# Performance work log

Hardware: AMD Instinct MI355X
Metric: run time of the kernel (lower is better)

Reference implementation:

```python
import jax, jax.numpy as jnp
import numpy as np

N = 50000      # nodes
E = 1600000    # edges (before self loops)
IN = 128       # in_channels
HID = 64       # hidden_channels
HEADS = 2
NEG_SLOPE = 0.2  # PyG GATConv default


def setup_inputs() -> dict:
    key = jax.random.key(0)
    ks = jax.random.split(key, 12)
    s = 0.05
    return {
        "x": jax.random.normal(ks[0], (N, IN), jnp.float32),
        "edge_index": jax.random.randint(ks[1], (2, E), 0, N, dtype=jnp.int32),
        # layer 1: GATConv(IN -> HID, heads=HEADS, concat=True)
        "W1": jax.random.normal(ks[2], (IN, HEADS * HID), jnp.float32) * s,
        "a_src1": jax.random.normal(ks[3], (HEADS, HID), jnp.float32) * s,
        "a_dst1": jax.random.normal(ks[4], (HEADS, HID), jnp.float32) * s,
        "b1": jax.random.normal(ks[5], (HEADS * HID,), jnp.float32) * s,
        # layer 2: GATConv(HEADS*HID -> HID, heads=1, concat=False)
        "W2": jax.random.normal(ks[6], (HEADS * HID, HID), jnp.float32) * s,
        "a_src2": jax.random.normal(ks[7], (1, HID), jnp.float32) * s,
        "a_dst2": jax.random.normal(ks[8], (1, HID), jnp.float32) * s,
        "b2": jax.random.normal(ks[9], (HID,), jnp.float32) * s,
        "lin_w": jax.random.normal(ks[10], (HID, 1), jnp.float32) * s,
        "lin_b": jax.random.normal(ks[11], (1,), jnp.float32) * s,
    }


def gat_layer(x, src, dst, W, a_src, a_dst, b, heads, out_ch, concat, n):
    # linear transform: [n, heads, out_ch]
    h = (x @ W).reshape(n, heads, out_ch)
    # per-node attention logit halves  [n, heads]
    al_src = jnp.sum(h * a_src, axis=-1)
    al_dst = jnp.sum(h * a_dst, axis=-1)
    # per-edge logits (gather) + LeakyReLU  [e, heads]
    e = jax.nn.leaky_relu(al_src[src] + al_dst[dst], negative_slope=NEG_SLOPE)
    # segment softmax over edges grouped by destination node
    m = jax.ops.segment_max(e, dst, num_segments=n)
    ex = jnp.exp(e - m[dst])
    denom = jax.ops.segment_sum(ex, dst, num_segments=n)
    alpha = ex / (denom[dst] + 1e-16)
    # weighted message scatter-add  [n, heads, out_ch]
    out = jax.ops.segment_sum(h[src] * alpha[:, :, None], dst, num_segments=n)
    out = out.reshape(n, heads * out_ch) if concat else out.mean(axis=1)
    return out + b


def reference(x, edge_index, W1, a_src1, a_dst1, b1, W2, a_src2, a_dst2, b2, lin_w, lin_b):
    # PyG GATConv adds self loops by default
    loops = jnp.arange(N, dtype=edge_index.dtype)
    src = jnp.concatenate([edge_index[0], loops])
    dst = jnp.concatenate([edge_index[1], loops])
    h = gat_layer(x, src, dst, W1, a_src1, a_dst1, b1, HEADS, HID, True, N)
    h = jax.nn.elu(h)
    h = gat_layer(h, src, dst, W2, a_src2, a_dst2, b2, 1, HID, False, N)
    return (h @ lin_w + lin_b)[:, 0]  # squeeze(-1) -> [N]
```

## Files before the change

kernel.cpp:

```cpp
#include <hip/hip_runtime.h>
#include <hip/hip_fp16.h>


#define LEAKY(x) ((x) > 0.f ? (x) : 0.2f * (x))

typedef float v2f __attribute__((ext_vector_type(2)));
typedef _Float16 f16x8 __attribute__((ext_vector_type(8)));
typedef __fp16 h16x2 __attribute__((ext_vector_type(2)));
typedef float f32x4 __attribute__((ext_vector_type(4)));


template <int VPT>
__global__ __launch_bounds__(256) void bucket_cnt_kernel(const int* __restrict__ ei, int E, int n,
                                                         int* __restrict__ bc) {
  __shared__ int lc[256];
  int t = threadIdx.x;
  lc[t] = 0;
  __syncthreads();
  int base = blockIdx.x * (256 * VPT) + t;
  int tot = E + n;
#pragma unroll
  for (int u = 0; u < VPT; ++u) {
    int i = base + u * 256;
    if (i < tot) {
      int d = (i < E) ? ei[E + i] : (i - E);
      atomicAdd(&lc[d >> 8], 1);
    }
  }
  __syncthreads();
  if (lc[t]) atomicAdd(&bc[t], lc[t]);
}

__global__ __launch_bounds__(256) void bucket_scan_kernel(const int* __restrict__ bc,
                                                          int* __restrict__ boff,
                                                          int* __restrict__ bcur, int B,
                                                          int* __restrict__ off, int n, int Etot) {
  __shared__ int sm[256];
  int t = threadIdx.x;
  int v = (t < B) ? bc[t] : 0;
  sm[t] = v;
  __syncthreads();
  for (int s = 1; s < 256; s <<= 1) {
    int a = (t >= s) ? sm[t - s] : 0;
    __syncthreads();
    sm[t] += a;
    __syncthreads();
  }
  int excl = sm[t] - v;
  if (t < B) { boff[t] = excl; bcur[t] = excl; }
  if (t == 0) { boff[B] = Etot; off[n] = Etot; }
}

template <int VPT>
__global__ __launch_bounds__(256) void bucket_scatter_kernel(const int* __restrict__ ei, int E,
                                                             int n, int* __restrict__ bcur,
                                                             unsigned* __restrict__ entries) {
  __shared__ int lc[256];
  __shared__ int lbase[256];
  int t = threadIdx.x;
  lc[t] = 0;
  __syncthreads();
  int base = blockIdx.x * (256 * VPT) + t;
  int tot = E + n;
  int bb[VPT], ll[VPT];
  unsigned pk[VPT];
#pragma unroll
  for (int u = 0; u < VPT; ++u) {
    int i = base + u * 256;
    bb[u] = -1;
    if (i < tot) {
      int s, d;
      if (i < E) { s = ei[i]; d = ei[E + i]; }
      else       { s = d = i - E; }
      int b = d >> 8;
      bb[u] = b;
      ll[u] = atomicAdd(&lc[b], 1);
      pk[u] = (unsigned)s | ((unsigned)(d & 255) << 16);
    }
  }
  __syncthreads();
  if (lc[t]) lbase[t] = atomicAdd(&bcur[t], lc[t]);
  __syncthreads();
#pragma unroll
  for (int u = 0; u < VPT; ++u)
    if (bb[u] >= 0) entries[lbase[bb[u]] + ll[u]] = pk[u];
}

__global__ __launch_bounds__(256) void csr_build_kernel(const unsigned* __restrict__ entries,
                                                        const int* __restrict__ boff,
                                                        int* __restrict__ off,
                                                        unsigned* __restrict__ epair, int n) {
  __shared__ int hist[256];
  __shared__ int scn[256];
  __shared__ int cur[256];
  int b = blockIdx.x, t = threadIdx.x;
  int k0 = boff[b], k1 = boff[b + 1];
  hist[t] = 0;
  __syncthreads();
  for (int k = k0 + t; k < k1; k += 256) atomicAdd(&hist[(entries[k] >> 16) & 255], 1);
  __syncthreads();
  int v = hist[t];
  scn[t] = v;
  __syncthreads();
  for (int s = 1; s < 256; s <<= 1) {
    int a = (t >= s) ? scn[t - s] : 0;
    __syncthreads();
    scn[t] += a;
    __syncthreads();
  }
  int excl = scn[t] - v;
  int d = (b << 8) + t;
  if (d < n) off[d] = k0 + excl;
  cur[t] = k0 + excl;
  __syncthreads();
  unsigned dbase = (unsigned)(b << 8) << 16;
  for (int k = k0 + t; k < k1; k += 256) {
    unsigned e = entries[k];
    unsigned dl = (e >> 16) & 255;
    int p = atomicAdd(&cur[dl], 1);
    epair[p] = (e & 0xffffu) | (dbase + (dl << 16));
  }
}


__global__ __launch_bounds__(256) void wprep_kernel(const float* __restrict__ W1,
                                                    const float* __restrict__ W2,
                                                    const float* __restrict__ as2,
                                                    const float* __restrict__ ad2,
                                                    const float* __restrict__ lw,
                                                    unsigned short* __restrict__ Wp1,
                                                    float* __restrict__ vsrc2,
                                                    float* __restrict__ vdst2,
                                                    float* __restrict__ vlin) {
  int t = blockIdx.x * 256 + threadIdx.x;
  if (t < 16384) {
    int e = t;
    int i = e & 7;
    int c = (e >> 3) & 15;
    int g = (e >> 7) & 3;
    int kk = (e >> 9) & 3;
    int cn = e >> 11;
    int k = kk * 32 + g * 8 + i;
    int col = cn * 16 + c;
    __half h = __float2half(W1[k * 128 + col]);
    Wp1[e] = *(unsigned short*)&h;
  } else if (t < 16384 + 128) {
    int k = t - 16384;
    float a = 0.f, b = 0.f, s = 0.f;
    for (int cc = 0; cc < 64; ++cc) {
      float w = W2[k * 64 + cc];
      a = fmaf(w, as2[cc], a);
      b = fmaf(w, ad2[cc], b);
      s = fmaf(w, lw[cc], s);
    }
    vsrc2[k] = a;
    vdst2[k] = b;
    vlin[k] = s;
  }
}


__global__ __launch_bounds__(256) void gemm1_kernel(const float* __restrict__ X,
                                                    const uint4* __restrict__ Wp,
                                                    const float* __restrict__ a_src,
                                                    const float* __restrict__ a_dst,
                                                    unsigned char* __restrict__ Hout,
                                                    float2* __restrict__ als,
                                                    float2* __restrict__ ald, int n) {
  __shared__ float Xl[32 * 132];
  __shared__ float lgt[2][2][2][16];
  int t = threadIdx.x;
  int wave = t >> 6, lane = t & 63;
  int wm = wave >> 1, wn = wave & 1;
  int g = lane >> 4, c = lane & 15;
  int nb0 = blockIdx.x * 32;

  {
    const float4* Xg = (const float4*)X;
    float4* Xs = (float4*)Xl;
#pragma unroll
    for (int u = 0; u < 4; ++u) {
      int idx = u * 256 + t;
      int r = idx >> 5, c4 = idx & 31;
      int row = nb0 + r;
      int rc = row < n ? row : (n - 1);
      Xs[r * 33 + c4] = Xg[(size_t)rc * 32 + c4];
    }
  }
  __syncthreads();

  f16x8 af[4];
  const float* xr = Xl + (wm * 16 + c) * 132 + g * 8;
#pragma unroll
  for (int kk = 0; kk < 4; ++kk) {
    float4 x0 = *(const float4*)(xr + kk * 32);
    float4 x1 = *(const float4*)(xr + kk * 32 + 4);
    union { f16x8 v; h16x2 p[4]; } A;
    A.p[0] = __builtin_amdgcn_cvt_pkrtz(x0.x, x0.y);
    A.p[1] = __builtin_amdgcn_cvt_pkrtz(x0.z, x0.w);
    A.p[2] = __builtin_amdgcn_cvt_pkrtz(x1.x, x1.y);
    A.p[3] = __builtin_amdgcn_cvt_pkrtz(x1.z, x1.w);
    af[kk] = A.v;
  }

  f32x4 acc[4];
  f32x4 z = {0.f, 0.f, 0.f, 0.f};
#pragma unroll
  for (int cn = 0; cn < 4; ++cn) acc[cn] = z;
#pragma unroll
  for (int cn = 0; cn < 4; ++cn) {
    int cng = wn * 4 + cn;
#pragma unroll
    for (int kk = 0; kk < 4; ++kk) {
      union { uint4 u; f16x8 v; } B;
      B.u = Wp[(cng * 4 + kk) * 64 + lane];
      acc[cn] = __builtin_amdgcn_mfma_f32_16x16x32_f16(af[kk], B.v, acc[cn], 0, 0, 0);
    }
  }

  float asv[4], adv[4];
#pragma unroll
  for (int cn = 0; cn < 4; ++cn) {
    int col_l = wn * 64 + cn * 16 + c;
    asv[cn] = a_src[col_l];
    adv[cn] = a_dst[col_l];
  }
  float ps[4] = {0.f, 0.f, 0.f, 0.f};
  float pd[4] = {0.f, 0.f, 0.f, 0.f};
#pragma unroll
  for (int cn = 0; cn < 4; ++cn) {
#pragma unroll
    for (int r = 0; r < 4; ++r) {
      float v = acc[cn][r];
      ps[r] = fmaf(v, asv[cn], ps[r]);
      pd[r] = fmaf(v, adv[cn], pd[r]);
      int noder = nb0 + wm * 16 + g * 4 + r;
      int colg = wn * 64 + cn * 16 + c;
      if (noder < n) {
        int b8 = __builtin_amdgcn_cvt_pk_fp8_f32(v, v, 0, false);
        Hout[(size_t)noder * 128 + colg] = (unsigned char)(b8 & 0xff);
      }
    }
  }
#pragma unroll
  for (int r = 0; r < 4; ++r) {
#pragma unroll
    for (int m = 1; m <= 8; m <<= 1) {
      ps[r] += __shfl_xor(ps[r], m, 64);
      pd[r] += __shfl_xor(pd[r], m, 64);
    }
  }
  if (c == 0) {
#pragma unroll
    for (int r = 0; r < 4; ++r) {
      lgt[wm][wn][0][g * 4 + r] = ps[r];
      lgt[wm][wn][1][g * 4 + r] = pd[r];
    }
  }
  __syncthreads();
  if (t < 32) {
    int wmm = t >> 4, row = t & 15;
    int node = nb0 + wmm * 16 + row;
    if (node < n) {
      als[node] = make_float2(lgt[wmm][0][0][row], lgt[wmm][1][0][row]);
      ald[node] = make_float2(lgt[wmm][0][1][row], lgt[wmm][1][1][row]);
    }
  }
}


__global__ __launch_bounds__(256) void agg1_kernel(const unsigned char* __restrict__ Hb8,
                                                   const float2* __restrict__ als,
                                                   const float2* __restrict__ ald,
                                                   const unsigned* __restrict__ epair,
                                                   const int* __restrict__ off,
                                                   const float* __restrict__ b1,
                                                   const float* __restrict__ vsrc2,
                                                   const float* __restrict__ vdst2,
                                                   const float* __restrict__ vlin,
                                                   float2* __restrict__ gsrc,
                                                   float* __restrict__ adst2, int n) {
  __shared__ float wlds[4][128];
  int wid = (blockIdx.x * 256 + threadIdx.x) >> 6;
  int lane = threadIdx.x & 63;
  if (wid >= n) return;
  wid = __builtin_amdgcn_readfirstlane(wid);
  int wslot = (threadIdx.x >> 6) & 3;
  int half = lane >> 5;
  int k0 = off[wid], k1 = off[wid + 1];
  const unsigned short* Hu = (const unsigned short*)Hb8;
  float2 advv = ald[wid];
  float* wrow = &wlds[wslot][half << 6];

  float ax = 0.f, ay = 0.f, den = 0.f;

  for (int kb = k0; kb < k1; kb += 64) {
    int rem = min(k1 - kb, 64);
    int e = kb + (lane < rem ? lane : rem - 1);
    unsigned pp = epair[e];
    float2 l = als[pp & 0xffffu];
    float g0 = __expf(LEAKY(l.x + advv.x));
    float g1 = __expf(LEAKY(l.y + advv.y));
    wlds[wslot][lane] = g0;
    wlds[wslot][64 + lane] = g1;

#define EDGE1(jj)                                                                   \
  {                                                                                 \
    unsigned p = ((unsigned)__builtin_amdgcn_readlane((int)pp, (jj))) & 0xffffu;    \
    float w = wrow[(jj)];                                                           \
    unsigned short hv = Hu[(p << 6) | (unsigned)lane];                              \
    v2f hf = __builtin_amdgcn_cvt_pk_f32_fp8((int)hv, false);                       \
    den += w;                                                                       \
    ax = fmaf(hf.x, w, ax);                                                         \
    ay = fmaf(hf.y, w, ay);                                                         \
  }

    int nb = rem >> 3;
    for (int b = 0; b < nb; ++b) {
      int jb = b << 3;
#pragma unroll
      for (int j = 0; j < 8; ++j) EDGE1(jb + j);
    }
    for (int jj = nb << 3; jj < rem; ++jj) EDGE1(jj);
#undef EDGE1
  }

  float inv = 1.f / (den + 1e-16f);
  float2 bv = ((const float2*)b1)[lane];
  float r0 = ax * inv + bv.x;
  float r1 = ay * inv + bv.y;
  r0 = r0 > 0.f ? r0 : (__expf(r0) - 1.f);
  r1 = r1 > 0.f ? r1 : (__expf(r1) - 1.f);
  float2 vs = ((const float2*)vsrc2)[lane];
  float2 vd = ((const float2*)vdst2)[lane];
  float2 vl = ((const float2*)vlin)[lane];
  float ps = r0 * vs.x + r1 * vs.y;
  float pd = r0 * vd.x + r1 * vd.y;
  float sv = r0 * vl.x + r1 * vl.y;
#pragma unroll
  for (int m = 1; m <= 32; m <<= 1) {
    ps += __shfl_xor(ps, m, 64);
    pd += __shfl_xor(pd, m, 64);
    sv += __shfl_xor(sv, m, 64);
  }
  if (lane == 0) {
    gsrc[wid] = make_float2(ps, sv);
    adst2[wid] = pd;
  }
}

__global__ __launch_bounds__(256) void agg2_kernel(const float2* __restrict__ gsrc,
                                                   const float* __restrict__ adst2,
                                                   const unsigned* __restrict__ epair,
                                                   const int* __restrict__ off,
                                                   const float* __restrict__ b2,
                                                   const float* __restrict__ lin_w,
                                                   const float* __restrict__ lin_b,
                                                   float* __restrict__ out, int n) {
  int wid = (blockIdx.x * 256 + threadIdx.x) >> 6;
  int lane = threadIdx.x & 63;
  if (wid >= n) return;
  wid = __builtin_amdgcn_readfirstlane(wid);
  int k0 = off[wid], k1 = off[wid + 1];
  float adv = adst2[wid];

  float num = 0.f, den = 0.f;
  for (int kb = k0; kb < k1; kb += 64) {
    int e = kb + lane;
    bool ok = e < k1;
    unsigned pp = epair[ok ? e : k0];
    float2 g = gsrc[pp & 0xffffu];
    float w = ok ? __expf(LEAKY(g.x + adv)) : 0.f;
    num = fmaf(w, g.y, num);
    den += w;
  }
  float bt = b2[lane] * lin_w[lane];
#pragma unroll
  for (int m = 1; m <= 32; m <<= 1) {
    num += __shfl_xor(num, m, 64);
    den += __shfl_xor(den, m, 64);
    bt  += __shfl_xor(bt, m, 64);
  }
  if (lane == 0) out[wid] = num / (den + 1e-16f) + bt + lin_b[0];
}


static inline size_t alignup(size_t v) { return (v + 255) & ~(size_t)255; }

extern "C" void kernel_launch(void* const* d_in, const int* in_sizes, int n_in,
                              void* d_out, int out_size, void* d_ws, size_t ws_size,
                              hipStream_t stream) {
  const float* x   = (const float*)d_in[0];
  const int*   ei  = (const int*)d_in[1];
  const float* W1  = (const float*)d_in[2];
  const float* as1 = (const float*)d_in[3];
  const float* ad1 = (const float*)d_in[4];
  const float* b1  = (const float*)d_in[5];
  const float* W2  = (const float*)d_in[6];
  const float* as2 = (const float*)d_in[7];
  const float* ad2 = (const float*)d_in[8];
  const float* b2  = (const float*)d_in[9];
  const float* lw  = (const float*)d_in[10];
  const float* lb  = (const float*)d_in[11];
  float* out = (float*)d_out;

  const int N = out_size;
  const int E = in_sizes[1] / 2;
  const int Etot = E + N;
  const int B = (N + 255) >> 8;

  char* p = (char*)d_ws;
  int* bcnt = (int*)p;  p += alignup((size_t)(B + 1) * 4);
  int* boff = (int*)p;  p += alignup((size_t)(B + 1) * 4);
  int* bcur = (int*)p;  p += alignup((size_t)B * 4);
  unsigned* entries = (unsigned*)p; p += alignup((size_t)Etot * 4);
  int* off  = (int*)p;  p += alignup((size_t)(N + 1) * 4);
  unsigned* epair = (unsigned*)p; p += alignup((size_t)Etot * 4);
  float2* als = (float2*)p; p += alignup((size_t)N * 8);
  float2* ald = (float2*)p; p += alignup((size_t)N * 8);
  float2* gsrc = (float2*)p; p += alignup((size_t)N * 8);
  float* adst2 = (float*)p; p += alignup((size_t)N * 4);
  unsigned char* h1b = (unsigned char*)p; p += alignup((size_t)N * 128);
  unsigned short* wp1 = (unsigned short*)p; p += alignup((size_t)16384 * 2);
  float* vsrc2 = (float*)p; p += alignup((size_t)128 * 4);
  float* vdst2 = (float*)p; p += alignup((size_t)128 * 4);
  float* vlin  = (float*)p; p += alignup((size_t)128 * 4);

  hipMemsetAsync(bcnt, 0, (size_t)(B + 1) * sizeof(int), stream);

  constexpr int VPT = 8;
  int egrid = (Etot + 256 * VPT - 1) / (256 * VPT);

  wprep_kernel<<<65, 256, 0, stream>>>(W1, W2, as2, ad2, lw, wp1, vsrc2, vdst2, vlin);
  bucket_cnt_kernel<VPT><<<egrid, 256, 0, stream>>>(ei, E, N, bcnt);
  bucket_scan_kernel<<<1, 256, 0, stream>>>(bcnt, boff, bcur, B, off, N, Etot);
  bucket_scatter_kernel<VPT><<<egrid, 256, 0, stream>>>(ei, E, N, bcur, entries);
  csr_build_kernel<<<B, 256, 0, stream>>>(entries, boff, off, epair, N);

  gemm1_kernel<<<(N + 31) / 32, 256, 0, stream>>>(
      x, (const uint4*)wp1, as1, ad1, h1b, als, ald, N);
  agg1_kernel<<<(N + 3) / 4, 256, 0, stream>>>(h1b, als, ald, epair, off, b1,
                                               vsrc2, vdst2, vlin, gsrc, adst2, N);
  agg2_kernel<<<(N + 3) / 4, 256, 0, stream>>>(gsrc, adst2, epair, off, b2, lw, lb, out, N);
}
```

Measured before the change: 152.7 us.

## Build CSR with global per-node atomics and 16-bit source indices

Replaces the two-level bucket sort (bucket count, bucket scatter, per-bucket CSR build) with a direct per-destination histogram using global atomics, a three-stage scan for offsets, and an atomic-cursor scatter. The edge list now stores only 16-bit source indices, which halves the edge array read by both aggregation kernels and removes one full pass over the edges. The cost is heavy contention on global atomics across about 1.65M edges spread over 50K counters, plus an extra launch. Edge order within each node becomes nondeterministic, which can change floating-point summation order.

```diff
diff --git a/kernel.cpp b/kernel.cpp
--- a/kernel.cpp
+++ b/kernel.cpp
@@ -11,33 +11,39 @@
 
 
 template <int VPT>
-__global__ __launch_bounds__(256) void bucket_cnt_kernel(const int* __restrict__ ei, int E, int n,
-                                                         int* __restrict__ bc) {
-  __shared__ int lc[256];
-  int t = threadIdx.x;
-  lc[t] = 0;
-  __syncthreads();
-  int base = blockIdx.x * (256 * VPT) + t;
+__global__ __launch_bounds__(256) void hist_kernel(const int* __restrict__ ei, int E, int n,
+                                                   int* __restrict__ cnt) {
+  int base = blockIdx.x * (256 * VPT) + threadIdx.x;
   int tot = E + n;
 #pragma unroll
   for (int u = 0; u < VPT; ++u) {
     int i = base + u * 256;
     if (i < tot) {
       int d = (i < E) ? ei[E + i] : (i - E);
-      atomicAdd(&lc[d >> 8], 1);
-    }
-  }
-  __syncthreads();
-  if (lc[t]) atomicAdd(&bc[t], lc[t]);
-}
-
-__global__ __launch_bounds__(256) void bucket_scan_kernel(const int* __restrict__ bc,
-                                                          int* __restrict__ boff,
-                                                          int* __restrict__ bcur, int B,
-                                                          int* __restrict__ off, int n, int Etot) {
+      atomicAdd(&cnt[d], 1);
+    }
+  }
+}
+
+__global__ __launch_bounds__(256) void bsum_kernel(const int* __restrict__ cnt,
+                                                   int* __restrict__ bsum, int n) {
   __shared__ int sm[256];
   int t = threadIdx.x;
-  int v = (t < B) ? bc[t] : 0;
+  int d = blockIdx.x * 256 + t;
+  sm[t] = (d < n) ? cnt[d] : 0;
+  __syncthreads();
+  for (int s = 128; s > 0; s >>= 1) {
+    if (t < s) sm[t] += sm[t + s];
+    __syncthreads();
+  }
+  if (t == 0) bsum[blockIdx.x] = sm[0];
+}
+
+__global__ __launch_bounds__(256) void scan196_kernel(const int* __restrict__ bsum,
+                                                      int* __restrict__ bbase, int B) {
+  __shared__ int sm[256];
+  int t = threadIdx.x;
+  int v = (t < B) ? bsum[t] : 0;
   sm[t] = v;
   __syncthreads();
   for (int s = 1; s < 256; s <<= 1) {
@@ -46,79 +52,49 @@
     sm[t] += a;
     __syncthreads();
   }
-  int excl = sm[t] - v;
-  if (t < B) { boff[t] = excl; bcur[t] = excl; }
-  if (t == 0) { boff[B] = Etot; off[n] = Etot; }
+  if (t < B) bbase[t] = sm[t] - v;
+}
+
+__global__ __launch_bounds__(256) void offs_kernel(const int* __restrict__ cnt,
+                                                   const int* __restrict__ bbase,
+                                                   int* __restrict__ off,
+                                                   int* __restrict__ cur, int n, int Etot) {
+  __shared__ int sm[256];
+  int t = threadIdx.x;
+  int d = blockIdx.x * 256 + t;
+  int v = (d < n) ? cnt[d] : 0;
+  sm[t] = v;
+  __syncthreads();
+  for (int s = 1; s < 256; s <<= 1) {
+    int a = (t >= s) ? sm[t - s] : 0;
+    __syncthreads();
+    sm[t] += a;
+    __syncthreads();
+  }
+  int pos = bbase[blockIdx.x] + sm[t] - v;
+  if (d < n) {
+    off[d] = pos;
+    cur[d] = pos;
+  }
+  if (d == n) off[n] = Etot;
 }
 
 template <int VPT>
-__global__ __launch_bounds__(256) void bucket_scatter_kernel(const int* __restrict__ ei, int E,
-                                                             int n, int* __restrict__ bcur,
-                                                             unsigned* __restrict__ entries) {
-  __shared__ int lc[256];
-  __shared__ int lbase[256];
-  int t = threadIdx.x;
-  lc[t] = 0;
-  __syncthreads();
-  int base = blockIdx.x * (256 * VPT) + t;
+__global__ __launch_bounds__(256) void scatter_kernel(const int* __restrict__ ei, int E, int n,
+                                                      int* __restrict__ cur,
+                                                      unsigned short* __restrict__ eps) {
+  int base = blockIdx.x * (256 * VPT) + threadIdx.x;
   int tot = E + n;
-  int bb[VPT], ll[VPT];
-  unsigned pk[VPT];
 #pragma unroll
   for (int u = 0; u < VPT; ++u) {
     int i = base + u * 256;
-    bb[u] = -1;
     if (i < tot) {
       int s, d;
       if (i < E) { s = ei[i]; d = ei[E + i]; }
       else       { s = d = i - E; }
-      int b = d >> 8;
-      bb[u] = b;
-      ll[u] = atomicAdd(&lc[b], 1);
-      pk[u] = (unsigned)s | ((unsigned)(d & 255) << 16);
-    }
-  }
-  __syncthreads();
-  if (lc[t]) lbase[t] = atomicAdd(&bcur[t], lc[t]);
-  __syncthreads();
-#pragma unroll
-  for (int u = 0; u < VPT; ++u)
-    if (bb[u] >= 0) entries[lbase[bb[u]] + ll[u]] = pk[u];
-}
-
-__global__ __launch_bounds__(256) void csr_build_kernel(const unsigned* __restrict__ entries,
-                                                        const int* __restrict__ boff,
-                                                        int* __restrict__ off,
-                                                        unsigned* __restrict__ epair, int n) {
-  __shared__ int hist[256];
-  __shared__ int scn[256];
-  __shared__ int cur[256];
-  int b = blockIdx.x, t = threadIdx.x;
-  int k0 = boff[b], k1 = boff[b + 1];
-  hist[t] = 0;
-  __syncthreads();
-  for (int k = k0 + t; k < k1; k += 256) atomicAdd(&hist[(entries[k] >> 16) & 255], 1);
-  __syncthreads();
-  int v = hist[t];
-  scn[t] = v;
-  __syncthreads();
-  for (int s = 1; s < 256; s <<= 1) {
-    int a = (t >= s) ? scn[t - s] : 0;
-    __syncthreads();
-    scn[t] += a;
-    __syncthreads();
-  }
-  int excl = scn[t] - v;
-  int d = (b << 8) + t;
-  if (d < n) off[d] = k0 + excl;
-  cur[t] = k0 + excl;
-  __syncthreads();
-  unsigned dbase = (unsigned)(b << 8) << 16;
-  for (int k = k0 + t; k < k1; k += 256) {
-    unsigned e = entries[k];
-    unsigned dl = (e >> 16) & 255;
-    int p = atomicAdd(&cur[dl], 1);
-    epair[p] = (e & 0xffffu) | (dbase + (dl << 16));
+      int p = atomicAdd(&cur[d], 1);
+      eps[p] = (unsigned short)s;
+    }
   }
 }
 
@@ -272,7 +248,7 @@
 __global__ __launch_bounds__(256) void agg1_kernel(const unsigned char* __restrict__ Hb8,
                                                    const float2* __restrict__ als,
                                                    const float2* __restrict__ ald,
-                                                   const unsigned* __restrict__ epair,
+                                                   const unsigned short* __restrict__ eps,
                                                    const int* __restrict__ off,
                                                    const float* __restrict__ b1,
                                                    const float* __restrict__ vsrc2,
@@ -297,8 +273,8 @@
   for (int kb = k0; kb < k1; kb += 64) {
     int rem = min(k1 - kb, 64);
     int e = kb + (lane < rem ? lane : rem - 1);
-    unsigned pp = epair[e];
-    float2 l = als[pp & 0xffffu];
+    unsigned pp = eps[e];
+    float2 l = als[pp];
     float g0 = __expf(LEAKY(l.x + advv.x));
     float g1 = __expf(LEAKY(l.y + advv.y));
     wlds[wslot][lane] = g0;
@@ -306,7 +282,7 @@
 
 #define EDGE1(jj)                                                                   \
   {                                                                                 \
-    unsigned p = ((unsigned)__builtin_amdgcn_readlane((int)pp, (jj))) & 0xffffu;    \
+    unsigned p = (unsigned)__builtin_amdgcn_readlane((int)pp, (jj));                \
     float w = wrow[(jj)];                                                           \
     unsigned short hv = Hu[(p << 6) | (unsigned)lane];                              \
     v2f hf = __builtin_amdgcn_cvt_pk_f32_fp8((int)hv, false);                       \
@@ -351,7 +327,7 @@
 
 __global__ __launch_bounds__(256) void agg2_kernel(const float2* __restrict__ gsrc,
                                                    const float* __restrict__ adst2,
-                                                   const unsigned* __restrict__ epair,
+                                                   const unsigned short* __restrict__ eps,
                                                    const int* __restrict__ off,
                                                    const float* __restrict__ b2,
                                                    const float* __restrict__ lin_w,
@@ -368,8 +344,8 @@
   for (int kb = k0; kb < k1; kb += 64) {
     int e = kb + lane;
     bool ok = e < k1;
-    unsigned pp = epair[ok ? e : k0];
-    float2 g = gsrc[pp & 0xffffu];
+    unsigned pp = eps[ok ? e : k0];
+    float2 g = gsrc[pp];
     float w = ok ? __expf(LEAKY(g.x + adv)) : 0.f;
     num = fmaf(w, g.y, num);
     den += w;
@@ -410,12 +386,12 @@
   const int B = (N + 255) >> 8;
 
   char* p = (char*)d_ws;
-  int* bcnt = (int*)p;  p += alignup((size_t)(B + 1) * 4);
-  int* boff = (int*)p;  p += alignup((size_t)(B + 1) * 4);
-  int* bcur = (int*)p;  p += alignup((size_t)B * 4);
-  unsigned* entries = (unsigned*)p; p += alignup((size_t)Etot * 4);
+  int* cnt  = (int*)p;  p += alignup((size_t)N * 4);
+  int* bsum = (int*)p;  p += alignup((size_t)(B + 1) * 4);
+  int* bbase= (int*)p;  p += alignup((size_t)(B + 1) * 4);
   int* off  = (int*)p;  p += alignup((size_t)(N + 1) * 4);
-  unsigned* epair = (unsigned*)p; p += alignup((size_t)Etot * 4);
+  int* cur  = (int*)p;  p += alignup((size_t)N * 4);
+  unsigned short* eps = (unsigned short*)p; p += alignup((size_t)Etot * 2);
   float2* als = (float2*)p; p += alignup((size_t)N * 8);
   float2* ald = (float2*)p; p += alignup((size_t)N * 8);
   float2* gsrc = (float2*)p; p += alignup((size_t)N * 8);
@@ -426,20 +402,21 @@
   float* vdst2 = (float*)p; p += alignup((size_t)128 * 4);
   float* vlin  = (float*)p; p += alignup((size_t)128 * 4);
 
-  hipMemsetAsync(bcnt, 0, (size_t)(B + 1) * sizeof(int), stream);
+  hipMemsetAsync(cnt, 0, (size_t)N * sizeof(int), stream);
 
   constexpr int VPT = 8;
   int egrid = (Etot + 256 * VPT - 1) / (256 * VPT);
 
   wprep_kernel<<<65, 256, 0, stream>>>(W1, W2, as2, ad2, lw, wp1, vsrc2, vdst2, vlin);
-  bucket_cnt_kernel<VPT><<<egrid, 256, 0, stream>>>(ei, E, N, bcnt);
-  bucket_scan_kernel<<<1, 256, 0, stream>>>(bcnt, boff, bcur, B, off, N, Etot);
-  bucket_scatter_kernel<VPT><<<egrid, 256, 0, stream>>>(ei, E, N, bcur, entries);
-  csr_build_kernel<<<B, 256, 0, stream>>>(entries, boff, off, epair, N);
+  hist_kernel<VPT><<<egrid, 256, 0, stream>>>(ei, E, N, cnt);
+  bsum_kernel<<<B, 256, 0, stream>>>(cnt, bsum, N);
+  scan196_kernel<<<1, 256, 0, stream>>>(bsum, bbase, B);
+  offs_kernel<<<B, 256, 0, stream>>>(cnt, bbase, off, cur, N, Etot);
+  scatter_kernel<VPT><<<egrid, 256, 0, stream>>>(ei, E, N, cur, eps);
 
   gemm1_kernel<<<(N + 31) / 32, 256, 0, stream>>>(
       x, (const uint4*)wp1, as1, ad1, h1b, als, ald, N);
-  agg1_kernel<<<(N + 3) / 4, 256, 0, stream>>>(h1b, als, ald, epair, off, b1,
+  agg1_kernel<<<(N + 3) / 4, 256, 0, stream>>>(h1b, als, ald, eps, off, b1,
                                                vsrc2, vdst2, vlin, gsrc, adst2, N);
-  agg2_kernel<<<(N + 3) / 4, 256, 0, stream>>>(gsrc, adst2, epair, off, b2, lw, lb, out, N);
-}
+  agg2_kernel<<<(N + 3) / 4, 256, 0, stream>>>(gsrc, adst2, eps, off, b2, lw, lb, out, N);
+}
```

New measurement: 295.9 us. +93.8%, slower.
